# Kernel optimization log

Hardware: AMD Instinct MI355X
Metric: run time of the kernel (lower is better)

The kernel has to match this reference:

```python
import jax, jax.numpy as jnp
import numpy as np

HEADS = 8
DIM_HEAD = 64
SCALE = DIM_HEAD ** -0.5


def setup_inputs() -> dict:
    key = jax.random.key(0)
    k1, k2, k3 = jax.random.split(key, 3)
    b, seq, dim = 4, 8192, 512
    inner = HEADS * DIM_HEAD  # 512
    x = jax.random.normal(k1, (b, seq, dim), dtype=jnp.float32)
    w_qkv = jax.random.normal(k2, (dim, 3 * inner), dtype=jnp.float32) * (dim ** -0.5)
    w_out = jax.random.normal(k3, (inner, dim), dtype=jnp.float32) * (inner ** -0.5)
    b_out = jnp.zeros((dim,), dtype=jnp.float32)
    return {"x": x, "w_qkv": w_qkv, "w_out": w_out, "b_out": b_out, "f": 32}


def reference(x, w_qkv, w_out, b_out, f):
    b, seq, dim = x.shape
    h, dh = HEADS, DIM_HEAD
    n_sp = seq // f  # spatial tokens per frame

    qkv = jnp.einsum('bnd,de->bne', x, w_qkv)  # [b, seq, 3*inner]
    q, k, v = jnp.split(qkv, 3, axis=-1)

    def to_axial(t):
        # 'b n (h d) -> (b h) n d' then 'b (f n) d -> (b f) n d'
        t = t.reshape(b, seq, h, dh).transpose(0, 2, 1, 3)  # [b, h, seq, dh]
        return t.reshape(b * h * f, n_sp, dh)               # [(b h f), n_sp, dh]

    q = to_axial(q) * SCALE
    k = to_axial(k)
    v = to_axial(v)

    sim = jnp.einsum('bid,bjd->bij', q, k)      # [(b h f), n_sp, n_sp]
    attn = jax.nn.softmax(sim, axis=-1)
    out = jnp.einsum('bij,bjd->bid', attn, v)   # [(b h f), n_sp, dh]

    # reverse: '(b f) n d -> b (f n) d' then '(b h) n d -> b n (h d)'
    out = out.reshape(b, h, seq, dh).transpose(0, 2, 1, 3).reshape(b, seq, h * dh)
    return jnp.einsum('bne,ed->bnd', out, w_out) + b_out
```

## Files before the change

### kernel.cpp

```cpp
#include <hip/hip_runtime.h>
#include <hip/hip_bf16.h>
#include <cstdint>

using bf16x8 = __attribute__((ext_vector_type(8))) short;
using f32x4  = __attribute__((ext_vector_type(4))) float;
using f32x16 = __attribute__((ext_vector_type(16))) float;

typedef const __attribute__((address_space(1))) void* gas_ptr;
typedef __attribute__((address_space(3))) void* lds_ptr;

#define M_ROWS 32768
#define PLANE ((size_t)M_ROWS * 64)

__device__ __forceinline__ short f2bf(float f) {
  unsigned u = __builtin_bit_cast(unsigned, f);
  u += 0x7fffu + ((u >> 16) & 1u);
  return (short)(u >> 16);
}

__device__ __forceinline__ unsigned pack2(float a, float b) {
  unsigned ua = __builtin_bit_cast(unsigned, a);
  ua += 0x7fffu + ((ua >> 16) & 1u);
  unsigned ub = __builtin_bit_cast(unsigned, b);
  ub += 0x7fffu + ((ub >> 16) & 1u);
  return (ua >> 16) | (ub & 0xffff0000u);
}

__global__ __launch_bounds__(256) void convert_bf16(const float* __restrict__ src,
                                                    short* __restrict__ dst, int n8) {
  for (int i = blockIdx.x * 256 + threadIdx.x; i < n8; i += gridDim.x * 256) {
    const float4* s = (const float4*)(src + (size_t)i * 8);
    float4 a = s[0], b = s[1];
    uint4 o;
    o.x = pack2(a.x, a.y); o.y = pack2(a.z, a.w);
    o.z = pack2(b.x, b.y); o.w = pack2(b.z, b.w);
    *(uint4*)(dst + (size_t)i * 8) = o;
  }
}

__global__ __launch_bounds__(256) void transpose_to_bf16(const float* __restrict__ src,
                                                         short* __restrict__ dst,
                                                         int R, int C) {
  int idx = blockIdx.x * 256 + threadIdx.x;
  if (idx >= R * C) return;
  int c = idx / R;
  int r = idx - c * R;
  dst[(size_t)c * R + r] = f2bf(src[(size_t)r * C + c]);
}

template <int MODE>
__device__ __forceinline__ void gemm8p_body(const short* __restrict__ A,
                                            const short* __restrict__ Bt,
                                            void* __restrict__ Cp,
                                            const float* __restrict__ bias,
                                            int Mt, int Nt, int N) {
  constexpr int K  = 512;
  constexpr int NT = K / 64;
  __shared__ short lds[65536];

  const int tid  = threadIdx.x;
  const int lane = tid & 63;
  const int w    = tid >> 6;
  const int c16  = lane & 15;
  const int g    = lane >> 4;
  const int wm   = w >> 2;
  const int wn   = w & 3;

  const int nwg = gridDim.x;
  const int bid = blockIdx.x;
  const int swz = (bid & 7) * (nwg >> 3) + (bid >> 3);
  const int mtile = swz / Nt;
  const int ntile = swz % Nt;
  const int m0 = mtile * 256;
  const int n0 = ntile * 256;

  const int stg_r = w * 16 + (lane >> 2);
  const int stg_c = ((lane & 3) ^ ((lane >> 3) & 3)) * 8;
  const short* gA = (MODE == 1)
      ? A + (size_t)(m0 + stg_r) * 64 + stg_c
      : A + (size_t)(m0 + stg_r) * K + stg_c;
  const short* gB = Bt + (size_t)(n0 + stg_r) * K + stg_c;
  short* const ldsA = lds;
  short* const ldsB = lds + 32768;
  const int stg_d = w * 512;

  const int f_lane = c16 * 32 + ((g ^ ((c16 >> 1) & 3)) * 8);

  f32x4 acc[2][4][4] = {};
  bf16x8 bf[4], af[4];

#define STG_(isA, p, kh, tile) do {                                               \
    short* _d = ((isA) ? ldsA : ldsB) + ((p) * 2 + (kh)) * 8192 + stg_d;          \
    if ((isA) && MODE == 1) {                                                     \
      const short* _s = gA + (size_t)(tile) * PLANE + (kh) * 32;                  \
      __builtin_amdgcn_global_load_lds((gas_ptr)_s, (lds_ptr)_d, 16, 0, 0);       \
      __builtin_amdgcn_global_load_lds((gas_ptr)(_s + 128 * 64), (lds_ptr)(_d + 4096), 16, 0, 0); \
    } else {                                                                      \
      const short* _s = ((isA) ? gA : gB) + (tile) * 64 + (kh) * 32;              \
      __builtin_amdgcn_global_load_lds((gas_ptr)_s, (lds_ptr)_d, 16, 0, 0);       \
      __builtin_amdgcn_global_load_lds((gas_ptr)(_s + 128 * K), (lds_ptr)(_d + 4096), 16, 0, 0); \
    }                                                                             \
  } while (0)

  STG_(1, 0, 0, 0); STG_(0, 0, 0, 0);
  STG_(1, 0, 1, 0); STG_(0, 0, 1, 0);
  STG_(1, 1, 0, 1); STG_(0, 1, 0, 1);
  asm volatile("s_waitcnt vmcnt(4)" ::: "memory");
  __builtin_amdgcn_s_barrier();
  asm volatile("" ::: "memory");

#define PHASE_(p, mq, kh, LOADB, sisA, sp, skh, stile, DOVM) do {                 \
    if (LOADB) {                                                                  \
      _Pragma("unroll")                                                           \
      for (int nf = 0; nf < 4; nf++)                                              \
        bf[nf] = *(const bf16x8*)&ldsB[((p) * 2 + (kh)) * 8192 +                  \
                                       (wn * 64 + nf * 16) * 32 + f_lane];        \
    }                                                                             \
    _Pragma("unroll")                                                             \
    for (int mf = 0; mf < 4; mf++)                                                \
      af[mf] = *(const bf16x8*)&ldsA[((p) * 2 + (kh)) * 8192 +                    \
                                     (wm * 128 + (mq) * 64 + mf * 16) * 32 + f_lane]; \
    STG_(sisA, sp, skh, stile);                                                   \
    asm volatile("" ::: "memory");                                                \
    __builtin_amdgcn_s_barrier();                                                 \
    __builtin_amdgcn_s_setprio(1);                                                \
    _Pragma("unroll")                                                             \
    for (int mf = 0; mf < 4; mf++)                                                \
      _Pragma("unroll")                                                           \
      for (int nf = 0; nf < 4; nf++)                                              \
        acc[mq][mf][nf] = __builtin_amdgcn_mfma_f32_16x16x32_bf16(af[mf], bf[nf], \
                                                      acc[mq][mf][nf], 0, 0, 0);  \
    __builtin_amdgcn_s_setprio(0);                                                \
    if (DOVM) asm volatile("s_waitcnt vmcnt(4)" ::: "memory");                    \
    asm volatile("" ::: "memory");                                                \
    __builtin_amdgcn_s_barrier();                                                 \
    asm volatile("" ::: "memory");                                                \
  } while (0)

  for (int j = 0; j < NT / 2; j++) {
    const int u  = 2 * j;
    const int t1 = u + 1;
    const int t2 = (u + 2 < NT) ? u + 2 : NT - 1;
    const int t3 = (u + 3 < NT) ? u + 3 : NT - 1;
    PHASE_(0, 0, 0, 1,  1, 1, 1, t1, 0);
    PHASE_(0, 1, 0, 0,  0, 1, 1, t1, 0);
    PHASE_(0, 0, 1, 1,  1, 0, 0, t2, 0);
    PHASE_(0, 1, 1, 0,  0, 0, 0, t2, 1);
    PHASE_(1, 0, 0, 1,  1, 0, 1, t2, 0);
    PHASE_(1, 1, 0, 0,  0, 0, 1, t2, 0);
    PHASE_(1, 0, 1, 1,  1, 1, 0, t3, 0);
    PHASE_(1, 1, 1, 0,  0, 1, 0, t3, 1);
  }
#undef PHASE_
#undef STG_

  asm volatile("s_waitcnt vmcnt(0)" ::: "memory");
  __builtin_amdgcn_s_barrier();

  if (MODE == 0) {
    #pragma unroll
    for (int mq = 0; mq < 2; mq++)
      #pragma unroll
      for (int mf = 0; mf < 4; mf++)
        #pragma unroll
        for (int nf = 0; nf < 4; nf++) {
          const int row = wm * 128 + mq * 64 + mf * 16 + g * 4;
          const int col = wn * 64 + nf * 16 + c16;
          #pragma unroll
          for (int r = 0; r < 4; r++) {
            const int rr = row + r;
            lds[rr * 256 + (col ^ (((rr >> 2) & 3) << 4))] = f2bf(acc[mq][mf][nf][r]);
          }
        }
    __syncthreads();
    #pragma unroll
    for (int cg = 0; cg < 4; cg++) {
      const int colbase = n0 + cg * 64;
      const int plane = (colbase >> 9) * 8 + ((colbase >> 6) & 7);
      short* op = (short*)Cp + (size_t)plane * PLANE + (size_t)m0 * 64;
      #pragma unroll
      for (int ps = 0; ps < 4; ps++) {
        const int row8 = ps * 64 + (tid >> 3);
        const int sc8  = (tid & 7) * 8;
        const int colL = cg * 64 + sc8;
        *(uint4*)(op + (size_t)row8 * 64 + sc8) =
            *(const uint4*)&lds[row8 * 256 + (colL ^ (((row8 >> 2) & 3) << 4))];
      }
    }
  } else {
    float* ldsf = (float*)lds;
    float* C = (float*)Cp;
    #pragma unroll
    for (int p = 0; p < 2; p++) {
      if (p) __syncthreads();
      #pragma unroll
      for (int mf = 0; mf < 4; mf++)
        #pragma unroll
        for (int nf = 0; nf < 4; nf++) {
          const int lrow = wm * 64 + mf * 16 + g * 4;
          const int col  = wn * 64 + nf * 16 + c16;
          const float bb = bias ? bias[n0 + col] : 0.f;
          #pragma unroll
          for (int r = 0; r < 4; r++) {
            const int rr = lrow + r;
            ldsf[rr * 256 + (col ^ (((rr >> 2) & 3) << 4))] = acc[p][mf][nf][r] + bb;
          }
        }
      __syncthreads();
      #pragma unroll
      for (int jj = 0; jj < 16; jj++) {
        const int lr   = jj * 8 + (tid >> 6);
        const int coff = (tid & 63) * 4;
        uint4 v = *(const uint4*)&ldsf[lr * 256 + (coff ^ (((lr >> 2) & 3) << 4))];
        const int grow = m0 + (lr >> 6) * 128 + p * 64 + (lr & 63);
        *(uint4*)&C[(size_t)grow * N + n0 + coff] = v;
      }
    }
  }
}

__global__ __launch_bounds__(512, 2) void gemm8p_qkv(const short* __restrict__ A,
                                                     const short* __restrict__ Bt,
                                                     void* __restrict__ Cp,
                                                     int Mt, int Nt, int N) {
  gemm8p_body<0>(A, Bt, Cp, nullptr, Mt, Nt, N);
}
__global__ __launch_bounds__(512, 2) void gemm8p_out(const short* __restrict__ A,
                                                     const short* __restrict__ Bt,
                                                     void* __restrict__ Cp,
                                                     const float* __restrict__ bias,
                                                     int Mt, int Nt, int N) {
  gemm8p_body<1>(A, Bt, Cp, bias, Mt, Nt, N);
}

__global__ __launch_bounds__(512, 2) void attn_kernel(const short* __restrict__ qkv,
                                                      short* __restrict__ attn_out) {
  __shared__ short Kl[256 * 64];
  __shared__ short Vr[256 * 64];

  const int tid    = threadIdx.x;
  const int lane   = tid & 63;
  const int w      = tid >> 6;
  const int lane31 = lane & 31;
  const int hi     = lane >> 5;

  const int bid = blockIdx.x;
  const int fr  = bid & 31;
  const int h   = (bid >> 5) & 7;
  const int bb  = bid >> 8;
  const size_t rowbase = (size_t)bb * 8192 + (size_t)fr * 256;
  const short* qp = qkv + (size_t)(0 + h) * PLANE + rowbase * 64;
  const short* kp = qkv + (size_t)(8 + h) * PLANE + rowbase * 64;
  const short* vp = qkv + (size_t)(16 + h) * PLANE + rowbase * 64;

  const int q0 = w * 32;

  const short* qrow = qp + (size_t)(q0 + lane31) * 64;
  bf16x8 qf[4];
  #pragma unroll
  for (int ds = 0; ds < 4; ds++)
    qf[ds] = *(const bf16x8*)(qrow + ds * 16 + 8 * hi);

  #pragma unroll
  for (int j = 0; j < 4; j++) {
    const int g  = j * 512 + tid;
    const int r  = g >> 3;
    const int sl = g & 7;
    const int off = r * 128 + ((sl ^ (r & 7)) << 4);
    uint4 kc = *(const uint4*)(kp + (size_t)g * 8);
    *(uint4*)((char*)Kl + off) = kc;
    uint4 vc = *(const uint4*)(vp + (size_t)g * 8);
    *(uint4*)((char*)Vr + off) = vc;
  }
  __syncthreads();

  {
    const int p   = tid & 127;
    const int grp = tid >> 7;
    const int r0 = 2 * p, r1 = 2 * p + 1;
    bf16x8 ta[2], tb[2];
    #pragma unroll
    for (int i = 0; i < 2; i++) {
      const int cb = grp * 32 + i * 16;
      ta[i] = *(const bf16x8*)((const char*)Vr + r0 * 128 + (cb ^ ((r0 & 7) << 4)));
      tb[i] = *(const bf16x8*)((const char*)Vr + r1 * 128 + (cb ^ ((r1 & 7) << 4)));
    }
    __syncthreads();
    #pragma unroll
    for (int i = 0; i < 2; i++) {
      #pragma unroll
      for (int k = 0; k < 8; k++) {
        const int d = grp * 16 + i * 8 + k;
        unsigned pk = ((unsigned)(unsigned short)ta[i][k]) |
                      (((unsigned)(unsigned short)tb[i][k]) << 16);
        *(unsigned*)((char*)Vr + d * 512 + ((4 * p) ^ ((d & 7) << 4))) = pk;
      }
    }
  }
  __syncthreads();

  const int swl = (lane31 & 7) << 4;
  unsigned pko[16];

  {
    f32x16 o0 = {}, o1 = {};
    float m = 0.f, l = 0.f;

    #pragma unroll
    for (int j = 0; j < 4; j++) {
      f32x16 sA = {}, sB = {};
      __builtin_amdgcn_s_setprio(1);
      #pragma unroll
      for (int ds = 0; ds < 4; ds++) {
        bf16x8 kfA = *(const bf16x8*)((const char*)Kl + (j * 64 + lane31) * 128 +
                                      ((ds * 32 + 16 * hi) ^ swl));
        sA = __builtin_amdgcn_mfma_f32_32x32x16_bf16(kfA, qf[ds], sA, 0, 0, 0);
        bf16x8 kfB = *(const bf16x8*)((const char*)Kl + (j * 64 + 32 + lane31) * 128 +
                                      ((ds * 32 + 16 * hi) ^ swl));
        sB = __builtin_amdgcn_mfma_f32_32x32x16_bf16(kfB, qf[ds], sB, 0, 0, 0);
      }
      __builtin_amdgcn_s_setprio(0);

      float tm[16];
      #pragma unroll
      for (int r = 0; r < 16; r++) tm[r] = fmaxf(sA[r], sB[r]);
      #pragma unroll
      for (int st = 8; st > 0; st >>= 1)
        #pragma unroll
        for (int r = 0; r < 8; r++)
          if (r < st) tm[r] = fmaxf(tm[r], tm[r + st]);
      float bm = fmaxf(tm[0], __shfl_xor(tm[0], 32));

      if (j == 0) {
        m = bm;
      } else if (!__all((bm - m) <= 64.f)) {
        const float mnew = fmaxf(m, bm);
        const float corr = __expf((m - mnew) * 0.125f);
        #pragma unroll
        for (int r = 0; r < 16; r++) { o0[r] *= corr; o1[r] *= corr; }
        l *= corr;
        m = mnew;
      }

      float ts[16];
      #pragma unroll
      for (int r = 0; r < 16; r++) {
        sA[r] = __expf((sA[r] - m) * 0.125f);
        sB[r] = __expf((sB[r] - m) * 0.125f);
        ts[r] = sA[r] + sB[r];
      }
      #pragma unroll
      for (int st = 8; st > 0; st >>= 1)
        #pragma unroll
        for (int r = 0; r < 8; r++)
          if (r < st) ts[r] += ts[r + st];
      l += ts[0] + __shfl_xor(ts[0], 32);

#define PVBLK(SV, rb, mm) do {                                                     \
        unsigned u0 = pack2(SV[(rb) + 0], SV[(rb) + 1]);                           \
        unsigned u1 = pack2(SV[(rb) + 2], SV[(rb) + 3]);                           \
        unsigned u2 = pack2(SV[(rb) + 4], SV[(rb) + 5]);                           \
        unsigned u3 = pack2(SV[(rb) + 6], SV[(rb) + 7]);                           \
        int s0 = hi ? (int)u0 : (int)u2;                                           \
        int s1 = hi ? (int)u1 : (int)u3;                                           \
        int r0 = __shfl_xor(s0, 32);                                               \
        int r1 = __shfl_xor(s1, 32);                                               \
        int4 paw;                                                                  \
        paw.x = hi ? r0 : (int)u0;                                                 \
        paw.y = hi ? r1 : (int)u1;                                                 \
        paw.z = hi ? (int)u2 : r0;                                                 \
        paw.w = hi ? (int)u3 : r1;                                                 \
        bf16x8 pa = __builtin_bit_cast(bf16x8, paw);                               \
        bf16x8 v0f = *(const bf16x8*)((const char*)Vr + (size_t)lane31 * 512 +     \
                                      (((mm) * 32 + 16 * hi) ^ swl));              \
        bf16x8 v1f = *(const bf16x8*)((const char*)Vr + (size_t)(32 + lane31) * 512 + \
                                      (((mm) * 32 + 16 * hi) ^ swl));              \
        o0 = __builtin_amdgcn_mfma_f32_32x32x16_bf16(v0f, pa, o0, 0, 0, 0);        \
        o1 = __builtin_amdgcn_mfma_f32_32x32x16_bf16(v1f, pa, o1, 0, 0, 0);        \
      } while (0)

      PVBLK(sA, 0, j * 4 + 0);
      PVBLK(sA, 8, j * 4 + 1);
      PVBLK(sB, 0, j * 4 + 2);
      PVBLK(sB, 8, j * 4 + 3);
#undef PVBLK
    }

    const float inv = 1.0f / l;
    #pragma unroll
    for (int r = 0; r < 16; r++) { o0[r] *= inv; o1[r] *= inv; }
    #pragma unroll
    for (int g2 = 0; g2 < 4; g2++) {
      pko[2 * g2 + 0] = pack2(o0[4 * g2 + 0], o0[4 * g2 + 1]);
      pko[2 * g2 + 1] = pack2(o0[4 * g2 + 2], o0[4 * g2 + 3]);
      pko[8 + 2 * g2 + 0] = pack2(o1[4 * g2 + 0], o1[4 * g2 + 1]);
      pko[8 + 2 * g2 + 1] = pack2(o1[4 * g2 + 2], o1[4 * g2 + 3]);
    }
  }

  __syncthreads();
  {
    const int row = q0 + lane31;
    const int rx  = (row & 7) << 4;
    #pragma unroll
    for (int g2 = 0; g2 < 4; g2++) {
      uint2 a, b;
      a.x = pko[2 * g2 + 0]; a.y = pko[2 * g2 + 1];
      b.x = pko[8 + 2 * g2 + 0]; b.y = pko[8 + 2 * g2 + 1];
      *(uint2*)((char*)Kl + row * 128 + ((16 * g2 + 8 * hi) ^ rx))      = a;
      *(uint2*)((char*)Kl + row * 128 + ((64 + 16 * g2 + 8 * hi) ^ rx)) = b;
    }
  }
  __syncthreads();
  short* op = attn_out + (size_t)h * PLANE + rowbase * 64;
  #pragma unroll
  for (int j = 0; j < 4; j++) {
    const int row = j * 64 + (tid >> 3);
    const int sl  = tid & 7;
    uint4 v = *(const uint4*)((const char*)Kl + row * 128 + ((sl << 4) ^ ((row & 7) << 4)));
    *(uint4*)(op + (size_t)row * 64 + sl * 8) = v;
  }
}

extern "C" void kernel_launch(void* const* d_in, const int* in_sizes, int n_in,
                              void* d_out, int out_size, void* d_ws, size_t ws_size,
                              hipStream_t stream) {
  const float* x     = (const float*)d_in[0];
  const float* w_qkv = (const float*)d_in[1];
  const float* w_out = (const float*)d_in[2];
  const float* b_out = (const float*)d_in[3];
  float* out = (float*)d_out;

  const int M = M_ROWS, DIM = 512, NQKV = 1536;

  short* wqkvT = (short*)d_ws;
  short* woutT = wqkvT + (size_t)NQKV * DIM;
  short* qkvb  = woutT + (size_t)DIM * DIM;
  short* attnb = qkvb + (size_t)M * NQKV;
  short* xbf   = attnb;

  transpose_to_bf16<<<(DIM * NQKV + 255) / 256, 256, 0, stream>>>(w_qkv, wqkvT, DIM, NQKV);
  transpose_to_bf16<<<(DIM * DIM + 255) / 256, 256, 0, stream>>>(w_out, woutT, DIM, DIM);
  convert_bf16<<<2048, 256, 0, stream>>>(x, xbf, M * DIM / 8);

  gemm8p_qkv<<<(M / 256) * (NQKV / 256), 512, 0, stream>>>(xbf, wqkvT, qkvb,
                                                           M / 256, NQKV / 256, NQKV);

  attn_kernel<<<1024, 512, 0, stream>>>(qkvb, attnb);

  gemm8p_out<<<(M / 256) * (DIM / 256), 512, 0, stream>>>(attnb, woutT, out, b_out,
                                                          M / 256, DIM / 256, DIM);
}
```

Baseline: 168.4 us.

## Fuse fp32-to-bf16 conversion of x into the QKV GEMM A-tile loads

Drops the separate convert_bf16 pass over x. The QKV GEMM now reads fp32 x directly into registers, packs it to bf16 and writes it into swizzled LDS, with A loads software-pipelined one phase ahead. This removes a full write and re-read of the bf16 copy of x, and one kernel launch. In exchange the GEMM reads twice the bytes for A, uses more VGPRs for the staged float4 values, and adds an lgkmcnt wait per A phase.

```diff
diff --git a/kernel.cpp b/kernel.cpp
--- a/kernel.cpp
+++ b/kernel.cpp
@@ -26,16 +26,11 @@
   return (ua >> 16) | (ub & 0xffff0000u);
 }
 
-__global__ __launch_bounds__(256) void convert_bf16(const float* __restrict__ src,
-                                                    short* __restrict__ dst, int n8) {
-  for (int i = blockIdx.x * 256 + threadIdx.x; i < n8; i += gridDim.x * 256) {
-    const float4* s = (const float4*)(src + (size_t)i * 8);
-    float4 a = s[0], b = s[1];
-    uint4 o;
-    o.x = pack2(a.x, a.y); o.y = pack2(a.z, a.w);
-    o.z = pack2(b.x, b.y); o.w = pack2(b.z, b.w);
-    *(uint4*)(dst + (size_t)i * 8) = o;
-  }
+__device__ __forceinline__ bf16x8 pk8(float4 a, float4 b) {
+  uint4 o;
+  o.x = pack2(a.x, a.y); o.y = pack2(a.z, a.w);
+  o.z = pack2(b.x, b.y); o.w = pack2(b.z, b.w);
+  return __builtin_bit_cast(bf16x8, o);
 }
 
 __global__ __launch_bounds__(256) void transpose_to_bf16(const float* __restrict__ src,
@@ -49,7 +44,8 @@
 }
 
 template <int MODE>
-__device__ __forceinline__ void gemm8p_body(const short* __restrict__ A,
+__device__ __forceinline__ void gemm8p_body(const float* __restrict__ Af,
+                                            const short* __restrict__ A,
                                             const short* __restrict__ Bt,
                                             void* __restrict__ Cp,
                                             const float* __restrict__ bias,
@@ -76,40 +72,49 @@
 
   const int stg_r = w * 16 + (lane >> 2);
   const int stg_c = ((lane & 3) ^ ((lane >> 3) & 3)) * 8;
-  const short* gA = (MODE == 1)
-      ? A + (size_t)(m0 + stg_r) * 64 + stg_c
-      : A + (size_t)(m0 + stg_r) * K + stg_c;
-  const short* gB = Bt + (size_t)(n0 + stg_r) * K + stg_c;
+  const float* gAf = Af ? (Af + (size_t)(m0 + stg_r) * K + (lane & 3) * 8) : nullptr;
+  const short* gA  = (MODE == 1) ? A + (size_t)(m0 + stg_r) * 64 + stg_c : nullptr;
+  const short* gB  = Bt + (size_t)(n0 + stg_r) * K + stg_c;
   short* const ldsA = lds;
   short* const ldsB = lds + 32768;
   const int stg_d = w * 512;
+  const int awz   = (lane & 3) ^ ((stg_r >> 1) & 3);
 
   const int f_lane = c16 * 32 + ((g ^ ((c16 >> 1) & 3)) * 8);
 
   f32x4 acc[2][4][4] = {};
   bf16x8 bf[4], af[4];
-
-#define STG_(isA, p, kh, tile) do {                                               \
-    short* _d = ((isA) ? ldsA : ldsB) + ((p) * 2 + (kh)) * 8192 + stg_d;          \
-    if ((isA) && MODE == 1) {                                                     \
-      const short* _s = gA + (size_t)(tile) * PLANE + (kh) * 32;                  \
-      __builtin_amdgcn_global_load_lds((gas_ptr)_s, (lds_ptr)_d, 16, 0, 0);       \
-      __builtin_amdgcn_global_load_lds((gas_ptr)(_s + 128 * 64), (lds_ptr)(_d + 4096), 16, 0, 0); \
-    } else {                                                                      \
-      const short* _s = ((isA) ? gA : gB) + (tile) * 64 + (kh) * 32;              \
-      __builtin_amdgcn_global_load_lds((gas_ptr)_s, (lds_ptr)_d, 16, 0, 0);       \
-      __builtin_amdgcn_global_load_lds((gas_ptr)(_s + 128 * K), (lds_ptr)(_d + 4096), 16, 0, 0); \
-    }                                                                             \
-  } while (0)
-
-  STG_(1, 0, 0, 0); STG_(0, 0, 0, 0);
-  STG_(1, 0, 1, 0); STG_(0, 0, 1, 0);
-  STG_(1, 1, 0, 1); STG_(0, 1, 0, 1);
-  asm volatile("s_waitcnt vmcnt(4)" ::: "memory");
-  __builtin_amdgcn_s_barrier();
-  asm volatile("" ::: "memory");
-
-#define PHASE_(p, mq, kh, LOADB, sisA, sp, skh, stile, DOVM) do {                 \
+  float4 aldA[4], aldB[4];
+
+#define STGB_(p, kh, tile) do {                                                   \
+    const short* _s = gB + (tile) * 64 + (kh) * 32;                               \
+    short* _d = ldsB + ((p) * 2 + (kh)) * 8192 + stg_d;                           \
+    __builtin_amdgcn_global_load_lds((gas_ptr)_s, (lds_ptr)_d, 16, 0, 0);         \
+    __builtin_amdgcn_global_load_lds((gas_ptr)(_s + 128 * K), (lds_ptr)(_d + 4096), 16, 0, 0); \
+  } while (0)
+
+#define STGA1_(p, kh, tile) do {                                                  \
+    const short* _s = gA + (size_t)(tile) * PLANE + (kh) * 32;                    \
+    short* _d = ldsA + ((p) * 2 + (kh)) * 8192 + stg_d;                           \
+    __builtin_amdgcn_global_load_lds((gas_ptr)_s, (lds_ptr)_d, 16, 0, 0);         \
+    __builtin_amdgcn_global_load_lds((gas_ptr)(_s + 128 * 64), (lds_ptr)(_d + 4096), 16, 0, 0); \
+  } while (0)
+
+#define ALOAD_(SET, tile, kh) do {                                                \
+    const float* _sf = gAf + (tile) * 64 + (kh) * 32;                             \
+    ald##SET[0] = *(const float4*)(_sf);                                          \
+    ald##SET[1] = *(const float4*)(_sf + 4);                                      \
+    ald##SET[2] = *(const float4*)(_sf + 128 * K);                                \
+    ald##SET[3] = *(const float4*)(_sf + 128 * K + 4);                            \
+  } while (0)
+
+#define AWRITE_(SET, wp, wkh) do {                                                \
+    short* _d0 = ldsA + ((wp) * 2 + (wkh)) * 8192 + stg_r * 32 + awz * 8;         \
+    *(bf16x8*)_d0          = pk8(ald##SET[0], ald##SET[1]);                       \
+    *(bf16x8*)(_d0 + 4096) = pk8(ald##SET[2], ald##SET[3]);                       \
+  } while (0)
+
+#define FRAG_(p, kh, mq, LOADB) do {                                              \
     if (LOADB) {                                                                  \
       _Pragma("unroll")                                                           \
       for (int nf = 0; nf < 4; nf++)                                              \
@@ -120,9 +125,9 @@
     for (int mf = 0; mf < 4; mf++)                                                \
       af[mf] = *(const bf16x8*)&ldsA[((p) * 2 + (kh)) * 8192 +                    \
                                      (wm * 128 + (mq) * 64 + mf * 16) * 32 + f_lane]; \
-    STG_(sisA, sp, skh, stile);                                                   \
-    asm volatile("" ::: "memory");                                                \
-    __builtin_amdgcn_s_barrier();                                                 \
+  } while (0)
+
+#define MFMA_(mq) do {                                                            \
     __builtin_amdgcn_s_setprio(1);                                                \
     _Pragma("unroll")                                                             \
     for (int mf = 0; mf < 4; mf++)                                                \
@@ -131,28 +136,101 @@
         acc[mq][mf][nf] = __builtin_amdgcn_mfma_f32_16x16x32_bf16(af[mf], bf[nf], \
                                                       acc[mq][mf][nf], 0, 0, 0);  \
     __builtin_amdgcn_s_setprio(0);                                                \
+  } while (0)
+
+#define APHASE_(p, kh, WSET, wp, wkh, LSET, ltile, lkh) do {                      \
+    FRAG_(p, kh, 0, 1);                                                           \
+    ALOAD_(LSET, ltile, lkh);                                                     \
+    AWRITE_(WSET, wp, wkh);                                                       \
+    asm volatile("s_waitcnt lgkmcnt(0)" ::: "memory");                            \
+    __builtin_amdgcn_s_barrier();                                                 \
+    MFMA_(0);                                                                     \
+    asm volatile("" ::: "memory");                                                \
+    __builtin_amdgcn_s_barrier();                                                 \
+    asm volatile("" ::: "memory");                                                \
+  } while (0)
+
+#define BPHASE_(p, kh, sp, skh, stile, DOVM) do {                                 \
+    FRAG_(p, kh, 1, 0);                                                           \
+    STGB_(sp, skh, stile);                                                        \
+    asm volatile("" ::: "memory");                                                \
+    __builtin_amdgcn_s_barrier();                                                 \
+    MFMA_(1);                                                                     \
+    if (DOVM) asm volatile("s_waitcnt vmcnt(6)" ::: "memory");                    \
+    asm volatile("" ::: "memory");                                                \
+    __builtin_amdgcn_s_barrier();                                                 \
+    asm volatile("" ::: "memory");                                                \
+  } while (0)
+
+#define PHASE1_(p, mq, kh, LOADB, sisA, sp, skh, stile, DOVM) do {                \
+    FRAG_(p, kh, mq, LOADB);                                                      \
+    if (sisA) STGA1_(sp, skh, stile); else STGB_(sp, skh, stile);                 \
+    asm volatile("" ::: "memory");                                                \
+    __builtin_amdgcn_s_barrier();                                                 \
+    MFMA_(mq);                                                                    \
     if (DOVM) asm volatile("s_waitcnt vmcnt(4)" ::: "memory");                    \
     asm volatile("" ::: "memory");                                                \
     __builtin_amdgcn_s_barrier();                                                 \
     asm volatile("" ::: "memory");                                                \
   } while (0)
 
-  for (int j = 0; j < NT / 2; j++) {
-    const int u  = 2 * j;
-    const int t1 = u + 1;
-    const int t2 = (u + 2 < NT) ? u + 2 : NT - 1;
-    const int t3 = (u + 3 < NT) ? u + 3 : NT - 1;
-    PHASE_(0, 0, 0, 1,  1, 1, 1, t1, 0);
-    PHASE_(0, 1, 0, 0,  0, 1, 1, t1, 0);
-    PHASE_(0, 0, 1, 1,  1, 0, 0, t2, 0);
-    PHASE_(0, 1, 1, 0,  0, 0, 0, t2, 1);
-    PHASE_(1, 0, 0, 1,  1, 0, 1, t2, 0);
-    PHASE_(1, 1, 0, 0,  0, 0, 1, t2, 0);
-    PHASE_(1, 0, 1, 1,  1, 1, 0, t3, 0);
-    PHASE_(1, 1, 1, 0,  0, 1, 0, t3, 1);
-  }
-#undef PHASE_
-#undef STG_
+  if (MODE == 0) {
+    ALOAD_(A, 0, 0);
+    ALOAD_(B, 0, 1);
+    STGB_(0, 0, 0); STGB_(0, 1, 0); STGB_(1, 0, 1);
+    AWRITE_(A, 0, 0);
+    AWRITE_(B, 0, 1);
+    ALOAD_(A, 1, 0);
+    asm volatile("s_waitcnt vmcnt(4) lgkmcnt(0)" ::: "memory");
+    __builtin_amdgcn_s_barrier();
+    asm volatile("" ::: "memory");
+
+    for (int j = 0; j < NT / 2; j++) {
+      const int u  = 2 * j;
+      const int t1 = u + 1;
+      const int t2 = (u + 2 < NT) ? u + 2 : NT - 1;
+      const int t3 = (u + 3 < NT) ? u + 3 : NT - 1;
+      APHASE_(0, 0, A, 1, 0, B, t1, 1);
+      BPHASE_(0, 0, 1, 1, t1, 0);
+      APHASE_(0, 1, B, 1, 1, A, t2, 0);
+      BPHASE_(0, 1, 0, 0, t2, 1);
+      APHASE_(1, 0, A, 0, 0, B, t2, 1);
+      BPHASE_(1, 0, 0, 1, t2, 0);
+      APHASE_(1, 1, B, 0, 1, A, t3, 0);
+      BPHASE_(1, 1, 1, 0, t3, 1);
+    }
+  } else {
+    STGA1_(0, 0, 0); STGB_(0, 0, 0);
+    STGA1_(0, 1, 0); STGB_(0, 1, 0);
+    STGA1_(1, 0, 1); STGB_(1, 0, 1);
+    asm volatile("s_waitcnt vmcnt(4)" ::: "memory");
+    __builtin_amdgcn_s_barrier();
+    asm volatile("" ::: "memory");
+
+    for (int j = 0; j < NT / 2; j++) {
+      const int u  = 2 * j;
+      const int t1 = u + 1;
+      const int t2 = (u + 2 < NT) ? u + 2 : NT - 1;
+      const int t3 = (u + 3 < NT) ? u + 3 : NT - 1;
+      PHASE1_(0, 0, 0, 1,  1, 1, 1, t1, 0);
+      PHASE1_(0, 1, 0, 0,  0, 1, 1, t1, 0);
+      PHASE1_(0, 0, 1, 1,  1, 0, 0, t2, 0);
+      PHASE1_(0, 1, 1, 0,  0, 0, 0, t2, 1);
+      PHASE1_(1, 0, 0, 1,  1, 0, 1, t2, 0);
+      PHASE1_(1, 1, 0, 0,  0, 0, 1, t2, 0);
+      PHASE1_(1, 0, 1, 1,  1, 1, 0, t3, 0);
+      PHASE1_(1, 1, 1, 0,  0, 1, 0, t3, 1);
+    }
+  }
+#undef APHASE_
+#undef BPHASE_
+#undef PHASE1_
+#undef FRAG_
+#undef MFMA_
+#undef STGB_
+#undef STGA1_
+#undef ALOAD_
+#undef AWRITE_
 
   asm volatile("s_waitcnt vmcnt(0)" ::: "memory");
   __builtin_amdgcn_s_barrier();
@@ -219,18 +297,18 @@
   }
 }
 
-__global__ __launch_bounds__(512, 2) void gemm8p_qkv(const short* __restrict__ A,
+__global__ __launch_bounds__(512, 2) void gemm8p_qkv(const float* __restrict__ Af,
                                                      const short* __restrict__ Bt,
                                                      void* __restrict__ Cp,
                                                      int Mt, int Nt, int N) {
-  gemm8p_body<0>(A, Bt, Cp, nullptr, Mt, Nt, N);
+  gemm8p_body<0>(Af, nullptr, Bt, Cp, nullptr, Mt, Nt, N);
 }
 __global__ __launch_bounds__(512, 2) void gemm8p_out(const short* __restrict__ A,
                                                      const short* __restrict__ Bt,
                                                      void* __restrict__ Cp,
                                                      const float* __restrict__ bias,
                                                      int Mt, int Nt, int N) {
-  gemm8p_body<1>(A, Bt, Cp, bias, Mt, Nt, N);
+  gemm8p_body<1>(nullptr, A, Bt, Cp, bias, Mt, Nt, N);
 }
 
 __global__ __launch_bounds__(512, 2) void attn_kernel(const short* __restrict__ qkv,
@@ -437,13 +515,11 @@
   short* woutT = wqkvT + (size_t)NQKV * DIM;
   short* qkvb  = woutT + (size_t)DIM * DIM;
   short* attnb = qkvb + (size_t)M * NQKV;
-  short* xbf   = attnb;
 
   transpose_to_bf16<<<(DIM * NQKV + 255) / 256, 256, 0, stream>>>(w_qkv, wqkvT, DIM, NQKV);
   transpose_to_bf16<<<(DIM * DIM + 255) / 256, 256, 0, stream>>>(w_out, woutT, DIM, DIM);
-  convert_bf16<<<2048, 256, 0, stream>>>(x, xbf, M * DIM / 8);
-
-  gemm8p_qkv<<<(M / 256) * (NQKV / 256), 512, 0, stream>>>(xbf, wqkvT, qkvb,
+
+  gemm8p_qkv<<<(M / 256) * (NQKV / 256), 512, 0, stream>>>(x, wqkvT, qkvb,
                                                            M / 256, NQKV / 256, NQKV);
 
   attn_kernel<<<1024, 512, 0, stream>>>(qkvb, attnb);
```

New measurement: 173.0 us. +2.8%, slower.
